# Kernel tuning notes

Hardware: AMD Instinct MI355X
Metric: run time of the kernel (lower is better)

The kernel has to match this reference:

```python
import jax, jax.numpy as jnp
import numpy as np

B, S, D = 8, 1024, 1024

def setup_inputs() -> dict:
    key = jax.random.key(0)
    k1, k2, k3, k4, k5 = jax.random.split(key, 5)
    head = jax.random.normal(k1, (B, S, D), dtype=jnp.float32)
    dep = jax.random.normal(k2, (B, S, D), dtype=jnp.float32)
    edge_U = jax.random.normal(k3, (D, D), dtype=jnp.float32) * (1.0 / np.sqrt(D))
    edge_W = jax.random.normal(k4, (1, 2 * D), dtype=jnp.float32) * (1.0 / np.sqrt(2 * D))
    edge_b = jax.random.normal(k5, (1,), dtype=jnp.float32)
    return {"head": head, "dep": dep, "edge_U": edge_U, "edge_W": edge_W, "edge_b": edge_b}

def reference(head, dep, edge_U, edge_W, edge_b):
    # t1[b,i,j] = head[b,i,:] @ edge_U @ dep[b,j,:]
    t1 = jnp.einsum('bid,dk,bjk->bij', head, edge_U, dep)
    # t2: original concatenates [head_i ; dep_j] for every (i,j) pair and applies
    # edge_W [1, 2D]. Algebraically t2[b,i,j] = head_i @ W[:D] + dep_j @ W[D:],
    # so we compute two [B,S] projections and broadcast-add (same math, no
    # O(B*S^2*2D) intermediate).
    d = head.shape[-1]
    w = edge_W[0]
    s_head = head @ w[:d]   # [B, S]
    s_dep = dep @ w[d:]     # [B, S]
    return t1 + s_head[:, :, None] + s_dep[:, None, :] + edge_b[0]
```

## Files before the change

### kernel.cpp

```cpp
#include <hip/hip_runtime.h>
#include <hip/hip_bf16.h>
#include <stdint.h>

#define D_DIM 1024
#define B_DIM 8
#define S_DIM 1024

typedef __bf16 bf16;
typedef __bf16 bf16x4 __attribute__((ext_vector_type(4)));
typedef __bf16 bf16x8 __attribute__((ext_vector_type(8)));
typedef float floatx4 __attribute__((ext_vector_type(4)));

__device__ __forceinline__ void async_copy16(const void* g, void* l) {
    __builtin_amdgcn_global_load_lds(
        (const __attribute__((address_space(1))) void*)g,
        (__attribute__((address_space(3))) void*)l, 16, 0, 0);
}

__global__ __launch_bounds__(256) void prep_du(
    const float* __restrict__ dep, const float* __restrict__ U,
    const float* __restrict__ edge_W,
    bf16* __restrict__ dep_b, bf16* __restrict__ U_b,
    float* __restrict__ s_dep)
{
    int blk  = blockIdx.x;
    int wid  = threadIdx.x >> 6;
    int lane = threadIdx.x & 63;

    if (blk < 1024) {
        const float* w2 = edge_W + D_DIM;
        #pragma unroll
        for (int rep = 0; rep < 2; ++rep) {
            int r = blk * 8 + wid * 2 + rep;
            const float* src = dep   + (size_t)r * D_DIM;
            bf16*        dst = dep_b + (size_t)r * D_DIM;
            float d = 0.0f;
            #pragma unroll
            for (int it = 0; it < 4; ++it) {
                int idx = it * 64 + lane;
                float4 v  = ((const float4*)src)[idx];
                float4 wv = ((const float4*)w2)[idx];
                bf16x4 o;
                o[0] = (bf16)v.x; o[1] = (bf16)v.y; o[2] = (bf16)v.z; o[3] = (bf16)v.w;
                ((bf16x4*)dst)[idx] = o;
                d += v.x * wv.x + v.y * wv.y + v.z * wv.z + v.w * wv.w;
            }
            #pragma unroll
            for (int off = 32; off > 0; off >>= 1)
                d += __shfl_down(d, off, 64);
            if (lane == 0) s_dep[r] = d;
        }
    } else {
        int row = (blk - 1024) * 4 + wid;
        const float* src = U   + (size_t)row * D_DIM;
        bf16*        dst = U_b + (size_t)row * D_DIM;
        #pragma unroll
        for (int it = 0; it < 4; ++it) {
            int idx = it * 64 + lane;
            float4 v = ((const float4*)src)[idx];
            bf16x4 o;
            o[0] = (bf16)v.x; o[1] = (bf16)v.y; o[2] = (bf16)v.z; o[3] = (bf16)v.w;
            ((bf16x4*)dst)[idx] = o;
        }
    }
}

__device__ __forceinline__ void gemm_core(
    const bf16* __restrict__ Ab, const bf16* __restrict__ Bb,
    bf16* As, bf16* Bs, floatx4 (&acc)[4][2],
    int wid, int lane, int quad, int l16, int wr, int wc)
{
    for (int k0 = 0; k0 < D_DIM; k0 += 64) {
        #pragma unroll
        for (int it = 0; it < 2; ++it) {
            int g  = wid * 128 + it * 64 + lane;
            int r  = g >> 3;
            int cg = (g & 7) ^ (r & 7);
            int ldsoff = (wid * 128 + it * 64) * 8;
            async_copy16(Ab + (size_t)r * D_DIM + k0 + cg * 8, &As[ldsoff]);
            async_copy16(Bb + (size_t)r * D_DIM + k0 + cg * 8, &Bs[ldsoff]);
        }
        __syncthreads();

        #pragma unroll
        for (int kk = 0; kk < 64; kk += 32) {
            bf16x8 a[4], b[2];
            #pragma unroll
            for (int mt = 0; mt < 4; ++mt) {
                int row  = wr * 64 + mt * 16 + l16;
                int slot = ((kk >> 3) + quad) ^ (row & 7);
                a[mt] = *(const bf16x8*)&As[row * 64 + slot * 8];
            }
            #pragma unroll
            for (int nt = 0; nt < 2; ++nt) {
                int row  = wc * 32 + nt * 16 + l16;
                int slot = ((kk >> 3) + quad) ^ (row & 7);
                b[nt] = *(const bf16x8*)&Bs[row * 64 + slot * 8];
            }
            __builtin_amdgcn_s_setprio(1);
            #pragma unroll
            for (int mt = 0; mt < 4; ++mt)
                #pragma unroll
                for (int nt = 0; nt < 2; ++nt)
                    acc[mt][nt] = __builtin_amdgcn_mfma_f32_16x16x32_bf16(
                        a[mt], b[nt], acc[mt][nt], 0, 0, 0);
            __builtin_amdgcn_s_setprio(0);
        }
        __syncthreads();
    }
}

__global__ __launch_bounds__(512) void gemm1_kernel(
    const bf16* __restrict__ dep_b, const bf16* __restrict__ U_b,
    bf16* __restrict__ tmpD,
    const float* __restrict__ head, const float* __restrict__ edge_W,
    bf16* __restrict__ head_b, float* __restrict__ s_head)
{
    int tid  = threadIdx.x;
    int wid  = tid >> 6;
    int lane = tid & 63;
    int lin  = blockIdx.x;

    if (lin % 3 != 0) {
        int c   = lin - lin / 3 - 1;
        int row = c * 8 + wid;
        const float* src = head   + (size_t)row * D_DIM;
        bf16*        dst = head_b + (size_t)row * D_DIM;
        const float* w1  = edge_W;
        float d = 0.0f;
        #pragma unroll
        for (int it = 0; it < 4; ++it) {
            int idx = it * 64 + lane;
            float4 v  = ((const float4*)src)[idx];
            float4 wv = ((const float4*)w1)[idx];
            bf16x4 o;
            o[0] = (bf16)v.x; o[1] = (bf16)v.y; o[2] = (bf16)v.z; o[3] = (bf16)v.w;
            ((bf16x4*)dst)[idx] = o;
            d += v.x * wv.x + v.y * wv.y + v.z * wv.z + v.w * wv.w;
        }
        #pragma unroll
        for (int off = 32; off > 0; off >>= 1)
            d += __shfl_down(d, off, 64);
        if (lane == 0) s_head[row] = d;
        return;
    }

    __shared__ bf16 As[128 * 64];
    __shared__ bf16 Bs[128 * 64];

    int quad = lane >> 4;
    int l16  = lane & 15;
    int wr   = wid >> 2;
    int wc   = wid & 3;

    int g  = lin / 3;
    int bx = g & 7;
    int by = g >> 3;

    int tile_m = by * 128;
    int tile_n = bx * 128;
    const bf16* Ab = dep_b + (size_t)tile_m * D_DIM;
    const bf16* Bb = U_b   + (size_t)tile_n * D_DIM;

    floatx4 zero = {0.0f, 0.0f, 0.0f, 0.0f};
    floatx4 acc[4][2];
    #pragma unroll
    for (int i = 0; i < 4; ++i)
        #pragma unroll
        for (int j = 0; j < 2; ++j) acc[i][j] = zero;

    gemm_core(Ab, Bb, As, Bs, acc, wid, lane, quad, l16, wr, wc);

    int row0 = tile_m + wr * 64;
    int col0 = tile_n + wc * 32;
    #pragma unroll
    for (int mt = 0; mt < 4; ++mt)
        #pragma unroll
        for (int r = 0; r < 4; ++r) {
            int row = row0 + mt * 16 + quad * 4 + r;
            #pragma unroll
            for (int nt = 0; nt < 2; ++nt) {
                int col = col0 + nt * 16 + l16;
                tmpD[(size_t)row * D_DIM + col] = (bf16)acc[mt][nt][r];
            }
        }
}

__global__ __launch_bounds__(512) void gemm2_kernel(
    const bf16* __restrict__ head_b, const bf16* __restrict__ tmpD,
    float* __restrict__ out,
    const float* __restrict__ s_head, const float* __restrict__ s_dep,
    const float* __restrict__ edge_b)
{
    __shared__ bf16 As[128 * 64];
    __shared__ bf16 Bs[128 * 64];

    int tid  = threadIdx.x;
    int wid  = tid >> 6;
    int lane = tid & 63;
    int quad = lane >> 4;
    int l16  = lane & 15;
    int wr   = wid >> 2;
    int wc   = wid & 3;

    int lin = blockIdx.x;
    int swz = (lin & 7) * 64 + (lin >> 3);
    int bx  = swz & 7;
    int by  = (swz >> 3) & 7;
    int bz  = swz >> 6;

    int tile_m = by * 128;
    int tile_n = bx * 128;
    const bf16* Ab = head_b + (size_t)bz * S_DIM * D_DIM + (size_t)tile_m * D_DIM;
    const bf16* Bb = tmpD   + (size_t)bz * S_DIM * D_DIM + (size_t)tile_n * D_DIM;

    floatx4 zero = {0.0f, 0.0f, 0.0f, 0.0f};
    floatx4 acc[4][2];
    #pragma unroll
    for (int i = 0; i < 4; ++i)
        #pragma unroll
        for (int j = 0; j < 2; ++j) acc[i][j] = zero;

    gemm_core(Ab, Bb, As, Bs, acc, wid, lane, quad, l16, wr, wc);

    float b0 = edge_b[0];
    const float* srow = s_head + (size_t)bz * S_DIM;
    const float* scol = s_dep  + (size_t)bz * S_DIM;
    float* Cf = out + (size_t)bz * S_DIM * S_DIM;
    int row0 = tile_m + wr * 64;
    int col0 = tile_n + wc * 32;
    #pragma unroll
    for (int mt = 0; mt < 4; ++mt)
        #pragma unroll
        for (int r = 0; r < 4; ++r) {
            int row = row0 + mt * 16 + quad * 4 + r;
            float sh = srow[row] + b0;
            #pragma unroll
            for (int nt = 0; nt < 2; ++nt) {
                int col = col0 + nt * 16 + l16;
                __builtin_nontemporal_store(acc[mt][nt][r] + sh + scol[col],
                                            &Cf[(size_t)row * S_DIM + col]);
            }
        }
}

extern "C" void kernel_launch(void* const* d_in, const int* in_sizes, int n_in,
                              void* d_out, int out_size, void* d_ws, size_t ws_size,
                              hipStream_t stream) {
    const float* head   = (const float*)d_in[0];
    const float* dep    = (const float*)d_in[1];
    const float* edge_U = (const float*)d_in[2];
    const float* edge_W = (const float*)d_in[3];
    const float* edge_b = (const float*)d_in[4];
    float* out = (float*)d_out;

    char* ws = (char*)d_ws;
    const size_t nBSD = (size_t)B_DIM * S_DIM * D_DIM;

    bf16*  head_b = (bf16*)ws;  ws += nBSD * sizeof(bf16);
    bf16*  dep_b  = (bf16*)ws;  ws += nBSD * sizeof(bf16);
    bf16*  U_b    = (bf16*)ws;  ws += (size_t)D_DIM * D_DIM * sizeof(bf16);
    bf16*  tmpD   = (bf16*)ws;  ws += nBSD * sizeof(bf16);
    float* s_head = (float*)ws; ws += (size_t)B_DIM * S_DIM * sizeof(float);
    float* s_dep  = (float*)ws; ws += (size_t)B_DIM * S_DIM * sizeof(float);

    prep_du<<<1024 + 256, 256, 0, stream>>>(
        dep, edge_U, edge_W, dep_b, U_b, s_dep);

    gemm1_kernel<<<1536, 512, 0, stream>>>(
        dep_b, U_b, tmpD, head, edge_W, head_b, s_head);

    gemm2_kernel<<<512, 512, 0, stream>>>(
        head_b, tmpD, out, s_head, s_dep, edge_b);
}
```

Measured before the change: 164.9 us.

## Halve GEMM block tile to 64x128 with 256-thread blocks

Result: no change. 166.6 us (+1.0%).

```diff
diff --git a/kernel.cpp b/kernel.cpp
--- a/kernel.cpp
+++ b/kernel.cpp
@@ -65,19 +65,26 @@
     }
 }
 
-__device__ __forceinline__ void gemm_core(
+__device__ __forceinline__ void gemm_core64(
     const bf16* __restrict__ Ab, const bf16* __restrict__ Bb,
     bf16* As, bf16* Bs, floatx4 (&acc)[4][2],
-    int wid, int lane, int quad, int l16, int wr, int wc)
+    int tid, int wid, int lane, int quad, int l16, int wc)
 {
     for (int k0 = 0; k0 < D_DIM; k0 += 64) {
         #pragma unroll
         for (int it = 0; it < 2; ++it) {
-            int g  = wid * 128 + it * 64 + lane;
+            int g  = it * 256 + tid;
             int r  = g >> 3;
             int cg = (g & 7) ^ (r & 7);
-            int ldsoff = (wid * 128 + it * 64) * 8;
+            int ldsoff = (it * 256 + wid * 64) * 8;
             async_copy16(Ab + (size_t)r * D_DIM + k0 + cg * 8, &As[ldsoff]);
+        }
+        #pragma unroll
+        for (int it = 0; it < 4; ++it) {
+            int g  = it * 256 + tid;
+            int r  = g >> 3;
+            int cg = (g & 7) ^ (r & 7);
+            int ldsoff = (it * 256 + wid * 64) * 8;
             async_copy16(Bb + (size_t)r * D_DIM + k0 + cg * 8, &Bs[ldsoff]);
         }
         __syncthreads();
@@ -87,7 +94,7 @@
             bf16x8 a[4], b[2];
             #pragma unroll
             for (int mt = 0; mt < 4; ++mt) {
-                int row  = wr * 64 + mt * 16 + l16;
+                int row  = mt * 16 + l16;
                 int slot = ((kk >> 3) + quad) ^ (row & 7);
                 a[mt] = *(const bf16x8*)&As[row * 64 + slot * 8];
             }
@@ -110,7 +117,7 @@
     }
 }
 
-__global__ __launch_bounds__(512) void gemm1_kernel(
+__global__ __launch_bounds__(256) void gemm1_kernel(
     const bf16* __restrict__ dep_b, const bf16* __restrict__ U_b,
     bf16* __restrict__ tmpD,
     const float* __restrict__ head, const float* __restrict__ edge_W,
@@ -121,43 +128,45 @@
     int lane = tid & 63;
     int lin  = blockIdx.x;
 
-    if (lin % 3 != 0) {
-        int c   = lin - lin / 3 - 1;
-        int row = c * 8 + wid;
-        const float* src = head   + (size_t)row * D_DIM;
-        bf16*        dst = head_b + (size_t)row * D_DIM;
-        const float* w1  = edge_W;
-        float d = 0.0f;
-        #pragma unroll
-        for (int it = 0; it < 4; ++it) {
-            int idx = it * 64 + lane;
-            float4 v  = ((const float4*)src)[idx];
-            float4 wv = ((const float4*)w1)[idx];
-            bf16x4 o;
-            o[0] = (bf16)v.x; o[1] = (bf16)v.y; o[2] = (bf16)v.z; o[3] = (bf16)v.w;
-            ((bf16x4*)dst)[idx] = o;
-            d += v.x * wv.x + v.y * wv.y + v.z * wv.z + v.w * wv.w;
-        }
-        #pragma unroll
-        for (int off = 32; off > 0; off >>= 1)
-            d += __shfl_down(d, off, 64);
-        if (lane == 0) s_head[row] = d;
+    if (lin & 1) {
+        int c = lin >> 1;
+        const float* w1 = edge_W;
+        #pragma unroll
+        for (int rep = 0; rep < 2; ++rep) {
+            int row = c * 8 + wid * 2 + rep;
+            const float* src = head   + (size_t)row * D_DIM;
+            bf16*        dst = head_b + (size_t)row * D_DIM;
+            float d = 0.0f;
+            #pragma unroll
+            for (int it = 0; it < 4; ++it) {
+                int idx = it * 64 + lane;
+                float4 v  = ((const float4*)src)[idx];
+                float4 wv = ((const float4*)w1)[idx];
+                bf16x4 o;
+                o[0] = (bf16)v.x; o[1] = (bf16)v.y; o[2] = (bf16)v.z; o[3] = (bf16)v.w;
+                ((bf16x4*)dst)[idx] = o;
+                d += v.x * wv.x + v.y * wv.y + v.z * wv.z + v.w * wv.w;
+            }
+            #pragma unroll
+            for (int off = 32; off > 0; off >>= 1)
+                d += __shfl_down(d, off, 64);
+            if (lane == 0) s_head[row] = d;
+        }
         return;
     }
 
-    __shared__ bf16 As[128 * 64];
+    __shared__ bf16 As[64 * 64];
     __shared__ bf16 Bs[128 * 64];
 
     int quad = lane >> 4;
     int l16  = lane & 15;
-    int wr   = wid >> 2;
-    int wc   = wid & 3;
-
-    int g  = lin / 3;
+    int wc   = wid;
+
+    int g  = lin >> 1;
     int bx = g & 7;
     int by = g >> 3;
 
-    int tile_m = by * 128;
+    int tile_m = by * 64;
     int tile_n = bx * 128;
     const bf16* Ab = dep_b + (size_t)tile_m * D_DIM;
     const bf16* Bb = U_b   + (size_t)tile_n * D_DIM;
@@ -169,15 +178,14 @@
         #pragma unroll
         for (int j = 0; j < 2; ++j) acc[i][j] = zero;
 
-    gemm_core(Ab, Bb, As, Bs, acc, wid, lane, quad, l16, wr, wc);
-
-    int row0 = tile_m + wr * 64;
+    gemm_core64(Ab, Bb, As, Bs, acc, tid, wid, lane, quad, l16, wc);
+
     int col0 = tile_n + wc * 32;
     #pragma unroll
     for (int mt = 0; mt < 4; ++mt)
         #pragma unroll
         for (int r = 0; r < 4; ++r) {
-            int row = row0 + mt * 16 + quad * 4 + r;
+            int row = tile_m + mt * 16 + quad * 4 + r;
             #pragma unroll
             for (int nt = 0; nt < 2; ++nt) {
                 int col = col0 + nt * 16 + l16;
@@ -186,13 +194,13 @@
         }
 }
 
-__global__ __launch_bounds__(512) void gemm2_kernel(
+__global__ __launch_bounds__(256) void gemm2_kernel(
     const bf16* __restrict__ head_b, const bf16* __restrict__ tmpD,
     float* __restrict__ out,
     const float* __restrict__ s_head, const float* __restrict__ s_dep,
     const float* __restrict__ edge_b)
 {
-    __shared__ bf16 As[128 * 64];
+    __shared__ bf16 As[64 * 64];
     __shared__ bf16 Bs[128 * 64];
 
     int tid  = threadIdx.x;
@@ -200,16 +208,15 @@
     int lane = tid & 63;
     int quad = lane >> 4;
     int l16  = lane & 15;
-    int wr   = wid >> 2;
-    int wc   = wid & 3;
+    int wc   = wid;
 
     int lin = blockIdx.x;
-    int swz = (lin & 7) * 64 + (lin >> 3);
+    int swz = (lin & 7) * 128 + (lin >> 3);
     int bx  = swz & 7;
-    int by  = (swz >> 3) & 7;
-    int bz  = swz >> 6;
-
-    int tile_m = by * 128;
+    int by  = (swz >> 3) & 15;
+    int bz  = swz >> 7;
+
+    int tile_m = by * 64;
     int tile_n = bx * 128;
     const bf16* Ab = head_b + (size_t)bz * S_DIM * D_DIM + (size_t)tile_m * D_DIM;
     const bf16* Bb = tmpD   + (size_t)bz * S_DIM * D_DIM + (size_t)tile_n * D_DIM;
@@ -221,19 +228,18 @@
         #pragma unroll
         for (int j = 0; j < 2; ++j) acc[i][j] = zero;
 
-    gemm_core(Ab, Bb, As, Bs, acc, wid, lane, quad, l16, wr, wc);
+    gemm_core64(Ab, Bb, As, Bs, acc, tid, wid, lane, quad, l16, wc);
 
     float b0 = edge_b[0];
     const float* srow = s_head + (size_t)bz * S_DIM;
     const float* scol = s_dep  + (size_t)bz * S_DIM;
     float* Cf = out + (size_t)bz * S_DIM * S_DIM;
-    int row0 = tile_m + wr * 64;
     int col0 = tile_n + wc * 32;
     #pragma unroll
     for (int mt = 0; mt < 4; ++mt)
         #pragma unroll
         for (int r = 0; r < 4; ++r) {
-            int row = row0 + mt * 16 + quad * 4 + r;
+            int row = tile_m + mt * 16 + quad * 4 + r;
             float sh = srow[row] + b0;
             #pragma unroll
             for (int nt = 0; nt < 2; ++nt) {
@@ -267,9 +273,9 @@
     prep_du<<<1024 + 256, 256, 0, stream>>>(
         dep, edge_U, edge_W, dep_b, U_b, s_dep);
 
-    gemm1_kernel<<<1536, 512, 0, stream>>>(
+    gemm1_kernel<<<2048, 256, 0, stream>>>(
         dep_b, U_b, tmpD, head, edge_W, head_b, s_head);
 
-    gemm2_kernel<<<512, 512, 0, stream>>>(
+    gemm2_kernel<<<1024, 256, 0, stream>>>(
         head_b, tmpD, out, s_head, s_dep, edge_b);
 }
```
